# Kernel optimization log

Measured on AMD Instinct MI355X. Metric: run time of the kernel, lower is better.

Reference implementation:

```python
import jax, jax.numpy as jnp
import numpy as np

N = 100000      # nodes
E = 800000      # edges (avg degree 8)
D_IN = 256      # input feature dim
D_H = 256       # hidden dim (hard-coded in module)
D_OUT = 128     # h_feats


def setup_inputs() -> dict:
    key = jax.random.key(0)
    ks = jax.random.split(key, 8)
    feat = jax.random.normal(ks[0], (N, D_IN), jnp.float32)
    src = jax.random.randint(ks[1], (E,), 0, N, dtype=jnp.int32)
    dst = jax.random.randint(ks[2], (E,), 0, N, dtype=jnp.int32)
    def lin(k, din, dout):
        return jax.random.normal(k, (din, dout), jnp.float32) / np.float32(np.sqrt(din))
    return {
        'feat': feat, 'src': src, 'dst': dst,
        'w_self1': lin(ks[3], D_IN, D_H), 'w_neigh1': lin(ks[4], D_IN, D_H),
        'b1': jnp.zeros((D_H,), jnp.float32),
        'w_self2': lin(ks[5], D_H, D_OUT), 'w_neigh2': lin(ks[6], D_H, D_OUT),
        'b2': jnp.zeros((D_OUT,), jnp.float32),
    }


def _sage_mean(h, src, dst, w_self, w_neigh, b):
    # DGL SAGEConv 'mean': rst = h @ W_self + mean_{in-neighbors}(h) @ W_neigh + b
    ones = jnp.ones((src.shape[0],), h.dtype)
    deg = jax.ops.segment_sum(ones, dst, num_segments=N)          # in-degree per node
    msum = jax.ops.segment_sum(h[src], dst, num_segments=N)      # [N, d] gather-scatter
    mean = msum / jnp.maximum(deg, 1.0)[:, None]                  # zero-degree -> 0
    return h @ w_self + mean @ w_neigh + b


def reference(feat, src, dst, w_self1, w_neigh1, b1, w_self2, w_neigh2, b2):
    h = jax.nn.relu(_sage_mean(feat, src, dst, w_self1, w_neigh1, b1))
    h = jax.nn.relu(_sage_mean(h, src, dst, w_self2, w_neigh2, b2))
    # F.normalize(h, dim=1): x / max(||x||_2, eps)
    norm = jnp.linalg.norm(h, axis=1, keepdims=True)
    return h / jnp.maximum(norm, 1e-12)
```

## Files before the change

### kernel.cpp

```cpp
#include <hip/hip_runtime.h>

#define DIN 256
#define DH  256
#define DOUT 128

typedef __attribute__((ext_vector_type(8))) short bf16x8;
typedef __attribute__((ext_vector_type(4))) float f32x4;
typedef __attribute__((ext_vector_type(2))) float f32x2;
typedef __attribute__((ext_vector_type(4))) unsigned short ushort4v;
typedef __attribute__((ext_vector_type(8))) unsigned short ushort8v;
typedef __attribute__((ext_vector_type(4))) unsigned int uint4v;

static __device__ __forceinline__ unsigned short f2bf(float x) {
    unsigned u = __float_as_uint(x);
    u += 0x7fffu + ((u >> 16) & 1u);
    return (unsigned short)(u >> 16);
}
static __device__ __forceinline__ float bf2f(unsigned short h) {
    return __uint_as_float(((unsigned)h) << 16);
}

static __device__ __forceinline__ void gload16(const unsigned short* g, void* l) {
    __builtin_amdgcn_global_load_lds(
        (const __attribute__((address_space(1))) unsigned int*)g,
        (__attribute__((address_space(3))) unsigned int*)l,
        16, 0, 0);
}

__global__ void prep_kernel(const float* __restrict__ feat, unsigned short* __restrict__ featb,
                            unsigned int* __restrict__ feat8, long long ncHalf,
                            const float* __restrict__ w_self1, const float* __restrict__ w_neigh1,
                            const float* __restrict__ w_self2, const float* __restrict__ w_neigh2,
                            unsigned short* __restrict__ ws1t, unsigned short* __restrict__ wn1t,
                            unsigned short* __restrict__ wcat,
                            const int* __restrict__ dst, int* __restrict__ cnt, int E,
                            int bCnt, int bWt) {
    int b = blockIdx.x;
    if (b < bCnt) {
        int e = b * 256 + threadIdx.x;
        if (e < E) atomicAdd(&cnt[dst[e]], 1);
    } else if (b < bCnt + bWt) {
        int idx = (b - bCnt) * 256 + threadIdx.x;
        if (idx < 65536) {
            int nn = idx >> 8, k = idx & 255;
            ws1t[idx] = f2bf(w_self1[k * 256 + nn]);
        } else if (idx < 131072) {
            int j = idx - 65536; int nn = j >> 8, k = j & 255;
            wn1t[j] = f2bf(w_neigh1[k * 256 + nn]);
        } else if (idx < 163840) {
            int j = idx - 131072; int nn = j >> 8, k = j & 255;
            wcat[j] = f2bf(w_neigh2[k * 128 + nn]);
        } else if (idx < 196608) {
            int j = idx - 163840; int nn = j >> 8, k = j & 255;
            wcat[32768 + j] = f2bf(w_self2[k * 128 + nn]);
        }
    } else {
        long long i = (b - bCnt - bWt) * 256LL + threadIdx.x;
        if (i >= ncHalf) return;
        long long i2 = i + ncHalf;
        f32x4 v0 = __builtin_nontemporal_load((const f32x4*)feat + i);
        f32x4 v1 = __builtin_nontemporal_load((const f32x4*)feat + i2);
        ushort4v o0, o1;
        o0[0] = f2bf(v0[0]); o0[1] = f2bf(v0[1]); o0[2] = f2bf(v0[2]); o0[3] = f2bf(v0[3]);
        o1[0] = f2bf(v1[0]); o1[1] = f2bf(v1[1]); o1[2] = f2bf(v1[2]); o1[3] = f2bf(v1[3]);
        *((ushort4v*)featb + i)  = o0;
        *((ushort4v*)featb + i2) = o1;
        int u0 = __builtin_amdgcn_cvt_pk_fp8_f32(v0[0], v0[1], 0, 0);
        u0     = __builtin_amdgcn_cvt_pk_fp8_f32(v0[2], v0[3], u0, 1);
        int u1 = __builtin_amdgcn_cvt_pk_fp8_f32(v1[0], v1[1], 0, 0);
        u1     = __builtin_amdgcn_cvt_pk_fp8_f32(v1[2], v1[3], u1, 1);
        feat8[i]  = (unsigned)u0;
        feat8[i2] = (unsigned)u1;
    }
}

__global__ void block_sums_kernel(const int* __restrict__ cnt, int* __restrict__ partial, int N) {
    __shared__ int sdata[256];
    int t = threadIdx.x;
    int base = blockIdx.x * 1024;
    int s = 0;
#pragma unroll
    for (int j = 0; j < 4; ++j) {
        int i = base + t * 4 + j;
        if (i < N) s += cnt[i];
    }
    sdata[t] = s; __syncthreads();
    for (int o = 128; o; o >>= 1) {
        if (t < o) sdata[t] += sdata[t + o];
        __syncthreads();
    }
    if (t == 0) partial[blockIdx.x] = sdata[0];
}

__global__ void scan_block_kernel(int* __restrict__ cnt, const int* __restrict__ partial,
                                  int* __restrict__ off, int N, int E, int nb) {
    __shared__ int sdata[256];
    __shared__ int pbase;
    int b = blockIdx.x, t = threadIdx.x;

    int pv = (t < nb) ? partial[t] : 0;
    sdata[t] = pv; __syncthreads();
    for (int o = 1; o < 256; o <<= 1) {
        int y = (t >= o) ? sdata[t - o] : 0;
        __syncthreads();
        sdata[t] += y;
        __syncthreads();
    }
    if (t == 0) pbase = (b == 0) ? 0 : sdata[b - 1];
    __syncthreads();
    int base0 = pbase;
    __syncthreads();

    int base = b * 1024;
    int vals[4]; int local = 0;
#pragma unroll
    for (int j = 0; j < 4; ++j) {
        int i = base + t * 4 + j;
        vals[j] = (i < N) ? cnt[i] : 0;
        local += vals[j];
    }
    sdata[t] = local; __syncthreads();
    for (int o = 1; o < 256; o <<= 1) {
        int y = (t >= o) ? sdata[t - o] : 0;
        __syncthreads();
        sdata[t] += y;
        __syncthreads();
    }
    int run = sdata[t] - local + base0;
#pragma unroll
    for (int j = 0; j < 4; ++j) {
        int i = base + t * 4 + j;
        if (i < N) { off[i] = run; cnt[i] = run; }
        run += vals[j];
    }
    if (b == 0 && t == 0) off[N] = E;
}

__global__ void fill_csr_kernel(const int* __restrict__ src, const int* __restrict__ dst,
                                int* __restrict__ cursor, int* __restrict__ csr, int E) {
    int e = blockIdx.x * blockDim.x + threadIdx.x;
    if (e < E) {
        int d = dst[e];
        int p = atomicAdd(&cursor[d], 1);
        csr[p] = src[e];
    }
}

__global__ void gather_mean256_kernel(const unsigned int* __restrict__ feat8, const int* __restrict__ off,
                                      const int* __restrict__ csr, unsigned short* __restrict__ agg, int N) {
    int wid  = (int)((blockIdx.x * (long long)blockDim.x + threadIdx.x) >> 6);
    int lane = threadIdx.x & 63;
    if (wid >= N) return;
    int start = off[wid], end = off[wid + 1];
    const int g   = lane >> 4;
    const int cl  = lane & 15;
    float a[16] = {};
    int e = start;
    for (; e + 7 < end; e += 8) {
        int s0 = csr[e + g], s1 = csr[e + 4 + g];
        uint4v v0 = *(const uint4v*)(feat8 + (long long)s0 * 64 + cl * 4);
        uint4v v1 = *(const uint4v*)(feat8 + (long long)s1 * 64 + cl * 4);
#pragma unroll
        for (int d = 0; d < 4; ++d) {
            f32x2 p0 = __builtin_amdgcn_cvt_pk_f32_fp8((int)v0[d], false);
            f32x2 p1 = __builtin_amdgcn_cvt_pk_f32_fp8((int)v0[d], true);
            f32x2 q0 = __builtin_amdgcn_cvt_pk_f32_fp8((int)v1[d], false);
            f32x2 q1 = __builtin_amdgcn_cvt_pk_f32_fp8((int)v1[d], true);
            a[d * 4 + 0] += p0[0] + q0[0];
            a[d * 4 + 1] += p0[1] + q0[1];
            a[d * 4 + 2] += p1[0] + q1[0];
            a[d * 4 + 3] += p1[1] + q1[1];
        }
    }
    for (; e < end; e += 4) {
        int idx = e + g;
        if (idx < end) {
            int s = csr[idx];
            uint4v v = *(const uint4v*)(feat8 + (long long)s * 64 + cl * 4);
#pragma unroll
            for (int d = 0; d < 4; ++d) {
                f32x2 p0 = __builtin_amdgcn_cvt_pk_f32_fp8((int)v[d], false);
                f32x2 p1 = __builtin_amdgcn_cvt_pk_f32_fp8((int)v[d], true);
                a[d * 4 + 0] += p0[0];
                a[d * 4 + 1] += p0[1];
                a[d * 4 + 2] += p1[0];
                a[d * 4 + 3] += p1[1];
            }
        }
    }
#pragma unroll
    for (int j = 0; j < 16; ++j) {
        a[j] += __shfl_xor(a[j], 16);
        a[j] += __shfl_xor(a[j], 32);
    }
    if (g == 0) {
        float inv = 1.0f / (float)max(end - start, 1);
        ushort8v o0, o1;
#pragma unroll
        for (int j = 0; j < 8; ++j) { o0[j] = f2bf(a[j] * inv); o1[j] = f2bf(a[8 + j] * inv); }
        unsigned short* dstp = agg + (long long)wid * 256 + cl * 16;
        *(ushort8v*)dstp       = o0;
        *(ushort8v*)(dstp + 8) = o1;
    }
}

__global__ __launch_bounds__(512)
void gemm1_kernel(const unsigned short* __restrict__ A,  const unsigned short* __restrict__ WT,
                  const unsigned short* __restrict__ A2, const unsigned short* __restrict__ WT2,
                  const float* __restrict__ bias, unsigned short* __restrict__ C, int M)
{
    const int K = 256;
    __shared__ __align__(16) char lds[2][24576];

    const int tid = threadIdx.x;
    const int wid = tid >> 6, lane = tid & 63;
    const int l15 = lane & 15, lg = lane >> 4;
    const int wr = wid >> 2, wc = wid & 3;
    const int row0 = blockIdx.x * 128;

    long long asrc; int adst;
    {
        int c = tid, r = c >> 2, s = c & 3;
        int kc = s ^ ((r >> 1) & 3);
        asrc = (long long)min(row0 + r, M - 1) * K + kc * 8;
        adst = c * 16;
    }
    long long bsrc[2]; int bdst[2];
#pragma unroll
    for (int i = 0; i < 2; ++i) {
        int c = wid * 128 + i * 64 + lane, r = c >> 2, s = c & 3;
        int kc = s ^ ((r >> 1) & 3);
        bsrc[i] = (long long)r * K + kc * 8;
        bdst[i] = 8192 + c * 16;
    }

    const int slot = (lg ^ ((l15 >> 1) & 3)) * 16;
    int aoff[4], boff[4];
#pragma unroll
    for (int m = 0; m < 4; ++m) aoff[m] = (wr * 64 + m * 16 + l15) * 64 + slot;
#pragma unroll
    for (int n = 0; n < 4; ++n) boff[n] = 8192 + (wc * 64 + n * 16 + l15) * 64 + slot;

    f32x4 acc[4][4] = {};

    auto stage = [&](int buf, int t) {
        const unsigned short* Ap = (t >= 8) ? A2 : A;
        const unsigned short* Wp = (t >= 8) ? WT2 : WT;
        int k0 = (t & 7) * 32;
        gload16(Ap + asrc + k0, &lds[buf][adst]);
        gload16(Wp + bsrc[0] + k0, &lds[buf][bdst[0]]);
        gload16(Wp + bsrc[1] + k0, &lds[buf][bdst[1]]);
    };

    stage(0, 0);
    __syncthreads();

    for (int t = 0; t < 16; ++t) {
        const int cur = t & 1;
        if (t + 1 < 16) stage(cur ^ 1, t + 1);
        const char* L = lds[cur];
        bf16x8 af[4], bfr[4];
#pragma unroll
        for (int m = 0; m < 4; ++m) af[m]  = *(const bf16x8*)(L + aoff[m]);
#pragma unroll
        for (int n = 0; n < 4; ++n) bfr[n] = *(const bf16x8*)(L + boff[n]);
#pragma unroll
        for (int m = 0; m < 4; ++m)
#pragma unroll
            for (int n = 0; n < 4; ++n)
                acc[m][n] = __builtin_amdgcn_mfma_f32_16x16x32_bf16(af[m], bfr[n], acc[m][n], 0, 0, 0);
        __syncthreads();
    }

#pragma unroll
    for (int m = 0; m < 4; ++m) {
#pragma unroll
        for (int rr = 0; rr < 4; ++rr) {
            int grow = row0 + wr * 64 + m * 16 + lg * 4 + rr;
            if (grow >= M) continue;
#pragma unroll
            for (int n = 0; n < 4; ++n) {
                int gcol = wc * 64 + n * 16 + l15;
                float v = fmaxf(acc[m][n][rr] + bias[gcol], 0.f);
                C[(long long)grow * 256 + gcol] = f2bf(v);
            }
        }
    }
}

__global__ __launch_bounds__(512)
void gemm23_kernel(const unsigned short* __restrict__ A, const unsigned short* __restrict__ WT,
                   const float* __restrict__ b2,
                   unsigned short* __restrict__ p2, unsigned short* __restrict__ self2, int M)
{
    const int K = 256;
    __shared__ __align__(16) char lds[2][24576];

    const int tid = threadIdx.x;
    const int wid = tid >> 6, lane = tid & 63;
    const int l15 = lane & 15, lg = lane >> 4;
    const int wr = wid >> 2, wc = wid & 3;
    const int row0 = blockIdx.x * 128;

    long long asrc; int adst;
    {
        int c = tid, r = c >> 2, s = c & 3;
        int kc = s ^ ((r >> 1) & 3);
        asrc = (long long)min(row0 + r, M - 1) * K + kc * 8;
        adst = c * 16;
    }
    long long bsrc[2]; int bdst[2];
#pragma unroll
    for (int i = 0; i < 2; ++i) {
        int c = wid * 128 + i * 64 + lane, r = c >> 2, s = c & 3;
        int kc = s ^ ((r >> 1) & 3);
        bsrc[i] = (long long)r * K + kc * 8;
        bdst[i] = 8192 + c * 16;
    }

    const int slot = (lg ^ ((l15 >> 1) & 3)) * 16;
    int aoff[4], boff[4];
#pragma unroll
    for (int m = 0; m < 4; ++m) aoff[m] = (wr * 64 + m * 16 + l15) * 64 + slot;
#pragma unroll
    for (int n = 0; n < 4; ++n) boff[n] = 8192 + (wc * 64 + n * 16 + l15) * 64 + slot;

    f32x4 acc[4][4] = {};

    auto stage = [&](int buf, int t) {
        int k0 = t * 32;
        gload16(A  + asrc + k0, &lds[buf][adst]);
        gload16(WT + bsrc[0] + k0, &lds[buf][bdst[0]]);
        gload16(WT + bsrc[1] + k0, &lds[buf][bdst[1]]);
    };

    stage(0, 0);
    __syncthreads();

    for (int t = 0; t < 8; ++t) {
        const int cur = t & 1;
        if (t + 1 < 8) stage(cur ^ 1, t + 1);
        const char* L = lds[cur];
        bf16x8 af[4], bfr[4];
#pragma unroll
        for (int m = 0; m < 4; ++m) af[m]  = *(const bf16x8*)(L + aoff[m]);
#pragma unroll
        for (int n = 0; n < 4; ++n) bfr[n] = *(const bf16x8*)(L + boff[n]);
#pragma unroll
        for (int m = 0; m < 4; ++m)
#pragma unroll
            for (int n = 0; n < 4; ++n)
                acc[m][n] = __builtin_amdgcn_mfma_f32_16x16x32_bf16(af[m], bfr[n], acc[m][n], 0, 0, 0);
        __syncthreads();
    }

    if (wc < 2) {
#pragma unroll
        for (int m = 0; m < 4; ++m)
#pragma unroll
            for (int rr = 0; rr < 4; ++rr) {
                int grow = row0 + wr * 64 + m * 16 + lg * 4 + rr;
                if (grow >= M) continue;
#pragma unroll
                for (int n = 0; n < 4; ++n) {
                    int col = wc * 64 + n * 16 + l15;
                    p2[(long long)grow * 128 + col] = f2bf(acc[m][n][rr]);
                }
            }
    } else {
        float bv[4];
#pragma unroll
        for (int n = 0; n < 4; ++n) bv[n] = b2[(wc - 2) * 64 + n * 16 + l15];
#pragma unroll
        for (int m = 0; m < 4; ++m)
#pragma unroll
            for (int rr = 0; rr < 4; ++rr) {
                int grow = row0 + wr * 64 + m * 16 + lg * 4 + rr;
                if (grow >= M) continue;
#pragma unroll
                for (int n = 0; n < 4; ++n) {
                    int col = (wc - 2) * 64 + n * 16 + l15;
                    self2[(long long)grow * 128 + col] = f2bf(acc[m][n][rr] + bv[n]);
                }
            }
    }
}

__global__ void gather_final_kernel(const unsigned short* __restrict__ p2, const int* __restrict__ off,
                                    const int* __restrict__ csr, const unsigned short* __restrict__ self2,
                                    float* __restrict__ out, int N) {
    int wid  = (int)((blockIdx.x * (long long)blockDim.x + threadIdx.x) >> 6);
    int lane = threadIdx.x & 63;
    if (wid >= N) return;
    int start = off[wid], end = off[wid + 1];
    const int g  = lane >> 4;
    const int c8 = (lane & 15) * 8;
    float a[8] = {};
    int e = start;
    for (; e + 7 < end; e += 8) {
        int s0 = csr[e + g], s1 = csr[e + 4 + g];
        ushort8v v0 = *(const ushort8v*)(p2 + (long long)s0 * 128 + c8);
        ushort8v v1 = *(const ushort8v*)(p2 + (long long)s1 * 128 + c8);
#pragma unroll
        for (int j = 0; j < 8; ++j) a[j] += bf2f(v0[j]) + bf2f(v1[j]);
    }
    for (; e < end; e += 4) {
        int idx = e + g;
        if (idx < end) {
            int s = csr[idx];
            ushort8v v = *(const ushort8v*)(p2 + (long long)s * 128 + c8);
#pragma unroll
            for (int j = 0; j < 8; ++j) a[j] += bf2f(v[j]);
        }
    }
#pragma unroll
    for (int j = 0; j < 8; ++j) {
        a[j] += __shfl_xor(a[j], 16);
        a[j] += __shfl_xor(a[j], 32);
    }
    float invd = 1.0f / (float)max(end - start, 1);
    ushort8v sv = *(const ushort8v*)(self2 + (long long)wid * 128 + c8);
    float v[8];
    float ss = 0.f;
#pragma unroll
    for (int j = 0; j < 8; ++j) {
        v[j] = fmaxf(bf2f(sv[j]) + a[j] * invd, 0.f);
        ss += v[j] * v[j];
    }
    ss += __shfl_xor(ss, 1);
    ss += __shfl_xor(ss, 2);
    ss += __shfl_xor(ss, 4);
    ss += __shfl_xor(ss, 8);
    float inv = 1.0f / fmaxf(sqrtf(ss), 1e-12f);
    if (g == 0) {
        f32x4 o0 = { v[0] * inv, v[1] * inv, v[2] * inv, v[3] * inv };
        f32x4 o1 = { v[4] * inv, v[5] * inv, v[6] * inv, v[7] * inv };
        float* dstp = out + (long long)wid * 128 + c8;
        __builtin_nontemporal_store(o0, (f32x4*)dstp);
        __builtin_nontemporal_store(o1, (f32x4*)(dstp + 4));
    }
}

extern "C" void kernel_launch(void* const* d_in, const int* in_sizes, int n_in,
                              void* d_out, int out_size, void* d_ws, size_t ws_size,
                              hipStream_t stream) {
    const float* feat     = (const float*)d_in[0];
    const int*   src      = (const int*)  d_in[1];
    const int*   dst      = (const int*)  d_in[2];
    const float* w_self1  = (const float*)d_in[3];
    const float* w_neigh1 = (const float*)d_in[4];
    const float* b1       = (const float*)d_in[5];
    const float* w_self2  = (const float*)d_in[6];
    const float* w_neigh2 = (const float*)d_in[7];
    const float* b2       = (const float*)d_in[8];
    float* out = (float*)d_out;

    const int N = in_sizes[0] / DIN;
    const int E = in_sizes[1];

    char* ws = (char*)d_ws;
    auto a4k = [](size_t x) { return (x + 4095) & ~(size_t)4095; };
    size_t o = 0;
    int* cnt  = (int*)(ws + o); o += a4k((size_t)N * 4);
    int* off  = (int*)(ws + o); o += a4k((size_t)(N + 1) * 4);
    int* part = (int*)(ws + o); o += a4k(1024);
    int* csr  = (int*)(ws + o); o += a4k((size_t)E * 4);
    unsigned short* ws1t = (unsigned short*)(ws + o); o += a4k((size_t)DIN * DH * 2);
    unsigned short* wn1t = (unsigned short*)(ws + o); o += a4k((size_t)DIN * DH * 2);
    unsigned short* wcat = (unsigned short*)(ws + o); o += a4k((size_t)256 * 256 * 2);
    unsigned int*   feat8 = (unsigned int*)(ws + o); o += a4k((size_t)N * DIN);
    unsigned short* featb = (unsigned short*)(ws + o); o += a4k((size_t)N * DIN * 2);
    unsigned short* aggb  = (unsigned short*)(ws + o); o += a4k((size_t)N * DIN * 2);
    unsigned short* h1b   = (unsigned short*)(ws + o); o += a4k((size_t)N * DH * 2);

    unsigned short* p2b    = featb;
    unsigned short* self2b = aggb;

    const int nblk = (N + 1023) / 1024;

    hipMemsetAsync(cnt, 0, (size_t)N * 4, stream);
    long long ncHalf = (long long)N * DIN / 8;
    const int bCnt = (E + 255) / 256;
    const int bWt  = 768;
    const int bCvt = (int)((ncHalf + 255) / 256);
    prep_kernel<<<bCnt + bWt + bCvt, 256, 0, stream>>>(
        feat, featb, feat8, ncHalf, w_self1, w_neigh1, w_self2, w_neigh2,
        ws1t, wn1t, wcat, dst, cnt, E, bCnt, bWt);

    block_sums_kernel<<<nblk, 256, 0, stream>>>(cnt, part, N);
    scan_block_kernel<<<nblk, 256, 0, stream>>>(cnt, part, off, N, E, nblk);
    fill_csr_kernel<<<(E + 255) / 256, 256, 0, stream>>>(src, dst, cnt, csr, E);

    const int mblk = (N + 127) / 128;

    gather_mean256_kernel<<<(N + 3) / 4, 256, 0, stream>>>(feat8, off, csr, aggb, N);
    gemm1_kernel<<<mblk, 512, 0, stream>>>(featb, ws1t, aggb, wn1t, b1, h1b, N);

    gemm23_kernel<<<mblk, 512, 0, stream>>>(h1b, wcat, b2, p2b, self2b, N);
    gather_final_kernel<<<(N + 3) / 4, 256, 0, stream>>>(p2b, off, csr, self2b, out, N);
}
```

Measured before the change: 282.5 us.

## Load fp32 features directly in gemm1 and drop bf16 feature copy

The prep kernel no longer writes a bf16 copy of the input features. gemm1 instead stages the fp32 features into LDS with a new swizzle and converts them to bf16 in registers with packed conversion instructions before the MFMA. This removes a 51 MB write and a 51 MB read of the bf16 copy, at the cost of gemm1 reading 102 MB of fp32 and needing more LDS per block. The p2b buffer is moved into the second half of aggb, and the nontemporal loads in prep become ordinary loads.

```diff
diff --git a/kernel.cpp b/kernel.cpp
--- a/kernel.cpp
+++ b/kernel.cpp
@@ -7,7 +7,6 @@
 typedef __attribute__((ext_vector_type(8))) short bf16x8;
 typedef __attribute__((ext_vector_type(4))) float f32x4;
 typedef __attribute__((ext_vector_type(2))) float f32x2;
-typedef __attribute__((ext_vector_type(4))) unsigned short ushort4v;
 typedef __attribute__((ext_vector_type(8))) unsigned short ushort8v;
 typedef __attribute__((ext_vector_type(4))) unsigned int uint4v;
 
@@ -20,14 +19,23 @@
     return __uint_as_float(((unsigned)h) << 16);
 }
 
-static __device__ __forceinline__ void gload16(const unsigned short* g, void* l) {
+static __device__ __forceinline__ void gload16(const void* g, void* l) {
     __builtin_amdgcn_global_load_lds(
         (const __attribute__((address_space(1))) unsigned int*)g,
         (__attribute__((address_space(3))) unsigned int*)l,
         16, 0, 0);
 }
 
-__global__ void prep_kernel(const float* __restrict__ feat, unsigned short* __restrict__ featb,
+static __device__ __forceinline__ bf16x8 cvt8bf(f32x4 lo, f32x4 hi) {
+    union { unsigned u[4]; bf16x8 v; } r;
+    asm("v_cvt_pk_bf16_f32 %0, %1, %2" : "=v"(r.u[0]) : "v"(lo[0]), "v"(lo[1]));
+    asm("v_cvt_pk_bf16_f32 %0, %1, %2" : "=v"(r.u[1]) : "v"(lo[2]), "v"(lo[3]));
+    asm("v_cvt_pk_bf16_f32 %0, %1, %2" : "=v"(r.u[2]) : "v"(hi[0]), "v"(hi[1]));
+    asm("v_cvt_pk_bf16_f32 %0, %1, %2" : "=v"(r.u[3]) : "v"(hi[2]), "v"(hi[3]));
+    return r.v;
+}
+
+__global__ void prep_kernel(const float* __restrict__ feat,
                             unsigned int* __restrict__ feat8, long long ncHalf,
                             const float* __restrict__ w_self1, const float* __restrict__ w_neigh1,
                             const float* __restrict__ w_self2, const float* __restrict__ w_neigh2,
@@ -58,13 +66,8 @@
         long long i = (b - bCnt - bWt) * 256LL + threadIdx.x;
         if (i >= ncHalf) return;
         long long i2 = i + ncHalf;
-        f32x4 v0 = __builtin_nontemporal_load((const f32x4*)feat + i);
-        f32x4 v1 = __builtin_nontemporal_load((const f32x4*)feat + i2);
-        ushort4v o0, o1;
-        o0[0] = f2bf(v0[0]); o0[1] = f2bf(v0[1]); o0[2] = f2bf(v0[2]); o0[3] = f2bf(v0[3]);
-        o1[0] = f2bf(v1[0]); o1[1] = f2bf(v1[1]); o1[2] = f2bf(v1[2]); o1[3] = f2bf(v1[3]);
-        *((ushort4v*)featb + i)  = o0;
-        *((ushort4v*)featb + i2) = o1;
+        f32x4 v0 = *((const f32x4*)feat + i);
+        f32x4 v1 = *((const f32x4*)feat + i2);
         int u0 = __builtin_amdgcn_cvt_pk_fp8_f32(v0[0], v0[1], 0, 0);
         u0     = __builtin_amdgcn_cvt_pk_fp8_f32(v0[2], v0[3], u0, 1);
         int u1 = __builtin_amdgcn_cvt_pk_fp8_f32(v1[0], v1[1], 0, 0);
@@ -205,12 +208,12 @@
 }
 
 __global__ __launch_bounds__(512)
-void gemm1_kernel(const unsigned short* __restrict__ A,  const unsigned short* __restrict__ WT,
+void gemm1_kernel(const float* __restrict__ featf, const unsigned short* __restrict__ WT,
                   const unsigned short* __restrict__ A2, const unsigned short* __restrict__ WT2,
                   const float* __restrict__ bias, unsigned short* __restrict__ C, int M)
 {
     const int K = 256;
-    __shared__ __align__(16) char lds[2][24576];
+    __shared__ __align__(16) char lds[2][32768];
 
     const int tid = threadIdx.x;
     const int wid = tid >> 6, lane = tid & 63;
@@ -218,12 +221,20 @@
     const int wr = wid >> 2, wc = wid & 3;
     const int row0 = blockIdx.x * 128;
 
-    long long asrc; int adst;
+    long long a1src[2]; int a1dst[2];
+#pragma unroll
+    for (int i = 0; i < 2; ++i) {
+        int c = tid + i * 512, r = c >> 3, s = c & 7;
+        int ss = s ^ ((r & 3) << 1);
+        a1src[i] = (long long)min(row0 + r, M - 1) * K + ss * 4;
+        a1dst[i] = c * 16;
+    }
+    long long a2src; int a2dst;
     {
         int c = tid, r = c >> 2, s = c & 3;
         int kc = s ^ ((r >> 1) & 3);
-        asrc = (long long)min(row0 + r, M - 1) * K + kc * 8;
-        adst = c * 16;
+        a2src = (long long)min(row0 + r, M - 1) * K + kc * 8;
+        a2dst = c * 16;
     }
     long long bsrc[2]; int bdst[2];
 #pragma unroll
@@ -231,25 +242,38 @@
         int c = wid * 128 + i * 64 + lane, r = c >> 2, s = c & 3;
         int kc = s ^ ((r >> 1) & 3);
         bsrc[i] = (long long)r * K + kc * 8;
-        bdst[i] = 8192 + c * 16;
-    }
-
+        bdst[i] = 16384 + c * 16;
+    }
+
+    int a1off[4];
+#pragma unroll
+    for (int m = 0; m < 4; ++m) {
+        int rl = wr * 64 + m * 16 + l15;
+        int s0 = (2 * lg) ^ ((rl & 3) << 1);
+        a1off[m] = rl * 128 + s0 * 16;
+    }
     const int slot = (lg ^ ((l15 >> 1) & 3)) * 16;
-    int aoff[4], boff[4];
-#pragma unroll
-    for (int m = 0; m < 4; ++m) aoff[m] = (wr * 64 + m * 16 + l15) * 64 + slot;
-#pragma unroll
-    for (int n = 0; n < 4; ++n) boff[n] = 8192 + (wc * 64 + n * 16 + l15) * 64 + slot;
+    int a2off[4], boff[4];
+#pragma unroll
+    for (int m = 0; m < 4; ++m) a2off[m] = (wr * 64 + m * 16 + l15) * 64 + slot;
+#pragma unroll
+    for (int n = 0; n < 4; ++n) boff[n] = 16384 + (wc * 64 + n * 16 + l15) * 64 + slot;
 
     f32x4 acc[4][4] = {};
 
     auto stage = [&](int buf, int t) {
-        const unsigned short* Ap = (t >= 8) ? A2 : A;
-        const unsigned short* Wp = (t >= 8) ? WT2 : WT;
-        int k0 = (t & 7) * 32;
-        gload16(Ap + asrc + k0, &lds[buf][adst]);
-        gload16(Wp + bsrc[0] + k0, &lds[buf][bdst[0]]);
-        gload16(Wp + bsrc[1] + k0, &lds[buf][bdst[1]]);
+        if (t < 8) {
+            int k0 = t * 32;
+            gload16(featf + a1src[0] + k0, &lds[buf][a1dst[0]]);
+            gload16(featf + a1src[1] + k0, &lds[buf][a1dst[1]]);
+            gload16(WT + bsrc[0] + k0, &lds[buf][bdst[0]]);
+            gload16(WT + bsrc[1] + k0, &lds[buf][bdst[1]]);
+        } else {
+            int k0 = (t - 8) * 32;
+            gload16(A2 + a2src + k0, &lds[buf][a2dst]);
+            gload16(WT2 + bsrc[0] + k0, &lds[buf][bdst[0]]);
+            gload16(WT2 + bsrc[1] + k0, &lds[buf][bdst[1]]);
+        }
     };
 
     stage(0, 0);
@@ -261,9 +285,18 @@
         const char* L = lds[cur];
         bf16x8 af[4], bfr[4];
 #pragma unroll
-        for (int m = 0; m < 4; ++m) af[m]  = *(const bf16x8*)(L + aoff[m]);
-#pragma unroll
         for (int n = 0; n < 4; ++n) bfr[n] = *(const bf16x8*)(L + boff[n]);
+        if (t < 8) {
+#pragma unroll
+            for (int m = 0; m < 4; ++m) {
+                f32x4 lo = *(const f32x4*)(L + a1off[m]);
+                f32x4 hi = *(const f32x4*)(L + a1off[m] + 16);
+                af[m] = cvt8bf(lo, hi);
+            }
+        } else {
+#pragma unroll
+            for (int m = 0; m < 4; ++m) af[m] = *(const bf16x8*)(L + a2off[m]);
+        }
 #pragma unroll
         for (int m = 0; m < 4; ++m)
 #pragma unroll
@@ -469,12 +502,11 @@
     unsigned short* wn1t = (unsigned short*)(ws + o); o += a4k((size_t)DIN * DH * 2);
     unsigned short* wcat = (unsigned short*)(ws + o); o += a4k((size_t)256 * 256 * 2);
     unsigned int*   feat8 = (unsigned int*)(ws + o); o += a4k((size_t)N * DIN);
-    unsigned short* featb = (unsigned short*)(ws + o); o += a4k((size_t)N * DIN * 2);
     unsigned short* aggb  = (unsigned short*)(ws + o); o += a4k((size_t)N * DIN * 2);
     unsigned short* h1b   = (unsigned short*)(ws + o); o += a4k((size_t)N * DH * 2);
 
-    unsigned short* p2b    = featb;
     unsigned short* self2b = aggb;
+    unsigned short* p2b    = aggb + (size_t)N * DOUT;
 
     const int nblk = (N + 1023) / 1024;
 
@@ -484,7 +516,7 @@
     const int bWt  = 768;
     const int bCvt = (int)((ncHalf + 255) / 256);
     prep_kernel<<<bCnt + bWt + bCvt, 256, 0, stream>>>(
-        feat, featb, feat8, ncHalf, w_self1, w_neigh1, w_self2, w_neigh2,
+        feat, feat8, ncHalf, w_self1, w_neigh1, w_self2, w_neigh2,
         ws1t, wn1t, wcat, dst, cnt, E, bCnt, bWt);
 
     block_sums_kernel<<<nblk, 256, 0, stream>>>(cnt, part, N);
@@ -494,7 +526,7 @@
     const int mblk = (N + 127) / 128;
 
     gather_mean256_kernel<<<(N + 3) / 4, 256, 0, stream>>>(feat8, off, csr, aggb, N);
-    gemm1_kernel<<<mblk, 512, 0, stream>>>(featb, ws1t, aggb, wn1t, b1, h1b, N);
+    gemm1_kernel<<<mblk, 512, 0, stream>>>(feat, ws1t, aggb, wn1t, b1, h1b, N);
 
     gemm23_kernel<<<mblk, 512, 0, stream>>>(h1b, wcat, b2, p2b, self2b, N);
     gather_final_kernel<<<(N + 3) / 4, 256, 0, stream>>>(p2b, off, csr, self2b, out, N);
```

Result: slower. 305.0 us (+8.0%).
